# Kernel tuning notes

Hardware: AMD Instinct MI355X
Metric: run time of the kernel (lower is better)

Reference implementation:

```python
import jax, jax.numpy as jnp
import numpy as np

N, IN_DIM, H, D = 4096, 512, 8, 64
NEG = -1e9  # additive mask value for non-edges


def setup_inputs() -> dict:
    key = jax.random.key(0)
    k1, k2, k3, k4, k5, k6 = jax.random.split(key, 6)
    data = jax.random.normal(k1, (N, IN_DIM), dtype=jnp.float32)
    r = jax.random.uniform(k2, (N, N), dtype=jnp.float32)
    connectivity = jnp.where(r < 0.05, 0.0, NEG).astype(jnp.float32)
    # xavier-uniform-ish init for params
    lim_w = float(np.sqrt(6.0 / (IN_DIM + H * D)))
    W = jax.random.uniform(k3, (H * D, IN_DIM), jnp.float32, -lim_w, lim_w)
    b = jnp.zeros((H * D,), jnp.float32)
    lim_p = float(np.sqrt(6.0 / (H * D + 1)))
    src_proj = jax.random.uniform(k4, (1, H, D), jnp.float32, -lim_p, lim_p)
    trg_proj = jax.random.uniform(k5, (1, H, D), jnp.float32, -lim_p, lim_p)
    return {"data": data, "connectivity": connectivity, "W": W, "b": b,
            "src_proj": src_proj, "trg_proj": trg_proj}


def reference(data, connectivity, W, b, src_proj, trg_proj):
    # dropout is identity in eval mode (reference is deterministic)
    data1 = (data @ W.T + b).reshape(N, H, D)          # (N,H,D)
    src = jnp.einsum('nhd,xhd->nh', data1, src_proj)   # (N,H)
    trg = jnp.einsum('nhd,xhd->nh', data1, trg_proj)   # (N,H)
    # scores: (H,N,1) + (H,1,N) broadcast outer-sum
    e = src.T[:, :, None] + trg.T[:, None, :]          # (H,N,N)
    e = jnp.where(e >= 0, e, 0.01 * e)                 # LeakyReLU(0.01)
    e = e + connectivity[None, :, :]                   # additive mask
    scores = jax.nn.softmax(e, axis=-1)                # (H,N,N)
    # bmm over heads: (H,N,N) x (H,N,D) -> (H,N,D)
    out = jnp.einsum('hnm,hmd->hnd', scores, data1.transpose(1, 0, 2))
    out = out.transpose(1, 0, 2).reshape(N, H * D)     # concat=True
    return out
```

## Files before the change

kernel.cpp:

```cpp
#include <hip/hip_runtime.h>
#include <hip/hip_bf16.h>

#define NN 4096
#define IN_DIM 512
#define NH 8
#define DD 64
#define HD 512
#define QCAP 128
#define RCAP 448


typedef __attribute__((ext_vector_type(8))) short short8;
typedef __attribute__((ext_vector_type(4))) float f32x4;
typedef __attribute__((ext_vector_type(2))) float f32x2;

static __device__ __forceinline__ unsigned short f2bf(float x) {
    __hip_bfloat16 h = __float2bfloat16(x);
    return *reinterpret_cast<unsigned short*>(&h);
}

__global__ __launch_bounds__(256) void k_cast2(const float* __restrict__ inA,
                                               unsigned short* __restrict__ outA,
                                               int n4A,
                                               const float* __restrict__ inB,
                                               unsigned short* __restrict__ outB,
                                               int n4B) {
    int t = blockIdx.x * 256 + threadIdx.x;
    const float* in;
    unsigned short* out;
    if (t < n4A) {
        in = inA; out = outA;
    } else {
        t -= n4A;
        if (t >= n4B) return;
        in = inB; out = outB;
    }
    float4 v = ((const float4*)in)[t];
    ushort4 o;
    o.x = f2bf(v.x); o.y = f2bf(v.y); o.z = f2bf(v.z); o.w = f2bf(v.w);
    ((ushort4*)out)[t] = o;
}

__global__ __launch_bounds__(256) void k_gemm_fused(const unsigned short* __restrict__ Ab,
                                                    const unsigned short* __restrict__ Wb,
                                                    const float* __restrict__ bias,
                                                    const float* __restrict__ sp,
                                                    const float* __restrict__ tp,
                                                    unsigned short* __restrict__ Cb,
                                                    float* __restrict__ src,
                                                    float* __restrict__ trg) {
    const int lane = threadIdx.x & 63;
    const int w = threadIdx.x >> 6;
    const int col = lane & 15;
    const int quad = lane >> 4;
    const int koff = quad * 8;
    const int h = blockIdx.x;
    const int m0 = h * 64;
    const int n0 = blockIdx.y * 64;

    const short8* ap  = (const short8*)(Ab + (size_t)(n0 + w * 16 + col) * IN_DIM + koff);
    const short8* bp0 = (const short8*)(Wb + (size_t)(m0 +  0 + col) * IN_DIM + koff);
    const short8* bp1 = (const short8*)(Wb + (size_t)(m0 + 16 + col) * IN_DIM + koff);
    const short8* bp2 = (const short8*)(Wb + (size_t)(m0 + 32 + col) * IN_DIM + koff);
    const short8* bp3 = (const short8*)(Wb + (size_t)(m0 + 48 + col) * IN_DIM + koff);

    f32x4 acc0 = {0.f, 0.f, 0.f, 0.f}, acc1 = acc0, acc2 = acc0, acc3 = acc0;

#pragma unroll 4
    for (int ks = 0; ks < 16; ks++) {
        short8 a  = ap[ks * 4];
        short8 b0 = bp0[ks * 4];
        short8 b1 = bp1[ks * 4];
        short8 b2 = bp2[ks * 4];
        short8 b3 = bp3[ks * 4];
        acc0 = __builtin_amdgcn_mfma_f32_16x16x32_bf16(a, b0, acc0, 0, 0, 0);
        acc1 = __builtin_amdgcn_mfma_f32_16x16x32_bf16(a, b1, acc1, 0, 0, 0);
        acc2 = __builtin_amdgcn_mfma_f32_16x16x32_bf16(a, b2, acc2, 0, 0, 0);
        acc3 = __builtin_amdgcn_mfma_f32_16x16x32_bf16(a, b3, acc3, 0, 0, 0);
    }

    const int rbase = n0 + w * 16 + quad * 4;
    f32x4 accs[4] = {acc0, acc1, acc2, acc3};
    float ps[4] = {0.f, 0.f, 0.f, 0.f};
    float pt[4] = {0.f, 0.f, 0.f, 0.f};
#pragma unroll
    for (int mt = 0; mt < 4; mt++) {
        const int m = m0 + mt * 16 + col;
        const float bv  = bias[m];
        const float spv = sp[m];
        const float tpv = tp[m];
#pragma unroll
        for (int r = 0; r < 4; r++) {
            float v = accs[mt][r] + bv;
            Cb[(size_t)(rbase + r) * HD + m] = f2bf(v);
            ps[r] += v * spv;
            pt[r] += v * tpv;
        }
    }
#pragma unroll
    for (int off = 1; off <= 8; off <<= 1) {
#pragma unroll
        for (int r = 0; r < 4; r++) {
            ps[r] += __shfl_xor(ps[r], off, 64);
            pt[r] += __shfl_xor(pt[r], off, 64);
        }
    }
    if (col < 4)
        src[(rbase + col) * 8 + h] = ps[col];
    else if (col < 8)
        trg[(rbase + col - 4) * 8 + h] = pt[col - 4];
}

__global__ __launch_bounds__(256) void k_rowattn(const float* __restrict__ conn,
                                                 const float* __restrict__ src,
                                                 const float* __restrict__ trg,
                                                 const unsigned short* __restrict__ d1b,
                                                 float* __restrict__ out) {
    __shared__ unsigned short seg[4][QCAP];
    __shared__ unsigned short elist[RCAP + 8];
    __shared__ int wcnt[4];
    __shared__ float cbuf[3][64][9];
    const int w = threadIdx.x >> 6, lane = threadIdx.x & 63;
    const int i = blockIdx.x;
    const int h = lane >> 3, d8 = lane & 7;

    const float* crow = conn + (size_t)i * NN + w * 1024;
    int cnt = 0;
#pragma unroll
    for (int c0 = 0; c0 < 1024; c0 += 256) {
        float4 c = *(const float4*)(crow + c0 + lane * 4);
        float cv[4] = {c.x, c.y, c.z, c.w};
#pragma unroll
        for (int q = 0; q < 4; q++) {
            bool edge = (cv[q] == 0.0f);
            unsigned long long mask = __ballot(edge);
            int pre = __popcll(mask & ((1ull << lane) - 1ull));
            int pos = cnt + pre;
            if (edge && pos < QCAP)
                seg[w][pos] = (unsigned short)(w * 1024 + c0 + lane * 4 + q);
            cnt += __popcll(mask);
        }
    }
    if (cnt > QCAP) cnt = QCAP;
    if (lane == 0) wcnt[w] = cnt;
    __syncthreads();

    const int c0n = wcnt[0], c1n = wcnt[1], c2n = wcnt[2], c3n = wcnt[3];
    int tot = c0n + c1n + c2n + c3n;
    if (tot > RCAP) tot = RCAP;
    const int base = (w == 0) ? 0 : (w == 1) ? c0n
                   : (w == 2) ? c0n + c1n : c0n + c1n + c2n;
    for (int k = lane; k < cnt && base + k < RCAP; k += 64)
        elist[base + k] = seg[w][k];
    __syncthreads();
    if (threadIdx.x < 4)
        elist[tot + threadIdx.x] = (tot > 0) ? elist[tot - 1] : (unsigned short)0;
    __syncthreads();

    const float sh = src[i * 8 + h];
    const unsigned voffB = (unsigned)(h * 64 + d8 * 8) * 2u;
    const unsigned toffB = (unsigned)h << 2;
    const unsigned char* vb = (const unsigned char*)d1b;
    const unsigned char* tb = (const unsigned char*)trg;
    const int kbeg = (tot * w) >> 2;
    const int kend = (tot * (w + 1)) >> 2;

    f32x2 a01 = {0.f, 0.f}, a23 = a01, a45 = a01, a67 = a01;
    float lsum = 0.f;
    if (kend > kbeg) {
        unsigned j0 = elist[kbeg];
        unsigned j1 = elist[kbeg + 1];
        unsigned j2 = elist[kbeg + 2];
        float t0 = *(const float*)(tb + (j0 << 5) + toffB);
        float t1 = *(const float*)(tb + (j1 << 5) + toffB);
        uint4 U0 = *(const uint4*)(vb + (j0 << 10) + voffB);
        uint4 U1 = *(const uint4*)(vb + (j1 << 10) + voffB);
#pragma unroll 3
        for (int k = kbeg; k < kend; k++) {
            unsigned j3 = elist[k + 3];
            float t2 = *(const float*)(tb + (j2 << 5) + toffB);
            uint4 U2 = *(const uint4*)(vb + (j2 << 10) + voffB);
            float e = sh + t0;
            e = fmaxf(e, 0.01f * e);
            float p = __expf(e);
            lsum += p;
            f32x2 p2 = {p, p};
            f32x2 v01 = {__uint_as_float(U0.x << 16), __uint_as_float(U0.x & 0xffff0000u)};
            f32x2 v23 = {__uint_as_float(U0.y << 16), __uint_as_float(U0.y & 0xffff0000u)};
            f32x2 v45 = {__uint_as_float(U0.z << 16), __uint_as_float(U0.z & 0xffff0000u)};
            f32x2 v67 = {__uint_as_float(U0.w << 16), __uint_as_float(U0.w & 0xffff0000u)};
            a01 += p2 * v01;
            a23 += p2 * v23;
            a45 += p2 * v45;
            a67 += p2 * v67;
            t0 = t1; t1 = t2;
            U0 = U1; U1 = U2;
            j2 = j3;
        }
    }

    float acc[8] = {a01.x, a01.y, a23.x, a23.y, a45.x, a45.y, a67.x, a67.y};
    if (w > 0) {
#pragma unroll
        for (int r = 0; r < 8; r++) cbuf[w - 1][lane][r] = acc[r];
        cbuf[w - 1][lane][8] = lsum;
    }
    __syncthreads();
    if (w == 0) {
#pragma unroll
        for (int wv = 0; wv < 3; wv++) {
#pragma unroll
            for (int r = 0; r < 8; r++) acc[r] += cbuf[wv][lane][r];
            lsum += cbuf[wv][lane][8];
        }
        float inv = (lsum > 0.f) ? (1.f / lsum) : 0.f;
        float* op = out + (size_t)i * HD + h * 64 + d8 * 8;
        *(float4*)op = make_float4(acc[0] * inv, acc[1] * inv, acc[2] * inv, acc[3] * inv);
        *(float4*)(op + 4) = make_float4(acc[4] * inv, acc[5] * inv, acc[6] * inv, acc[7] * inv);
    }
}

extern "C" void kernel_launch(void* const* d_in, const int* in_sizes, int n_in,
                              void* d_out, int out_size, void* d_ws, size_t ws_size,
                              hipStream_t stream) {
    const float* data = (const float*)d_in[0];
    const float* conn = (const float*)d_in[1];
    const float* W    = (const float*)d_in[2];
    const float* bias = (const float*)d_in[3];
    const float* sp   = (const float*)d_in[4];
    const float* tp   = (const float*)d_in[5];
    float* out = (float*)d_out;

    unsigned short* d1b = (unsigned short*)d_ws;
    unsigned short* Ab  = d1b + (size_t)NN * HD;
    unsigned short* Wb  = Ab + (size_t)NN * IN_DIM;
    float* src  = (float*)(Wb + (size_t)HD * IN_DIM);
    float* trg  = src + NN * NH;

    const int n4A = NN * IN_DIM / 4;
    const int n4B = HD * IN_DIM / 4;
    k_cast2<<<dim3((n4A + n4B + 255) / 256), 256, 0, stream>>>(data, Ab, n4A, W, Wb, n4B);
    k_gemm_fused<<<dim3(NH, NN / 64), 256, 0, stream>>>(Ab, Wb, bias, sp, tp, d1b, src, trg);
    k_rowattn<<<dim3(NN), 256, 0, stream>>>(conn, src, trg, d1b, out);
}
```

Baseline: 168.3 us.

## Overlap connectivity bitmask scan with projection GEMM in one launch

The scan of the dense connectivity matrix moves out of the attention kernel into extra workgroups of the GEMM launch, where it builds a per-row 64x64-bit edge bitmask. The 64 MB mask read can then run alongside the GEMM. The attention kernel rebuilds its edge list from the bitmask with a prefix scan and ctz loop in one wave, and the old per-wave QCAP truncation is gone. src/trg are prescaled by log2(e) so the inner loop can use a native exp2. The cost is an extra bitmask buffer in workspace and a serial ctz loop per lane.

```diff
diff --git a/kernel.cpp b/kernel.cpp
--- a/kernel.cpp
+++ b/kernel.cpp
@@ -6,8 +6,10 @@
 #define NH 8
 #define DD 64
 #define HD 512
-#define QCAP 128
 #define RCAP 448
+#define GEMM_WGS 512
+#define SCAN_WGS 1024
+#define LOG2E 1.4426950408889634f
 
 
 typedef __attribute__((ext_vector_type(8))) short short8;
@@ -41,22 +43,39 @@
     ((ushort4*)out)[t] = o;
 }
 
-__global__ __launch_bounds__(256) void k_gemm_fused(const unsigned short* __restrict__ Ab,
-                                                    const unsigned short* __restrict__ Wb,
-                                                    const float* __restrict__ bias,
-                                                    const float* __restrict__ sp,
-                                                    const float* __restrict__ tp,
-                                                    unsigned short* __restrict__ Cb,
-                                                    float* __restrict__ src,
-                                                    float* __restrict__ trg) {
+__global__ __launch_bounds__(256) void k_gemm_scan(const unsigned short* __restrict__ Ab,
+                                                   const unsigned short* __restrict__ Wb,
+                                                   const float* __restrict__ bias,
+                                                   const float* __restrict__ sp,
+                                                   const float* __restrict__ tp,
+                                                   const float* __restrict__ conn,
+                                                   unsigned short* __restrict__ Cb,
+                                                   float* __restrict__ src,
+                                                   float* __restrict__ trg,
+                                                   unsigned long long* __restrict__ bm) {
     const int lane = threadIdx.x & 63;
     const int w = threadIdx.x >> 6;
+
+    if (blockIdx.x >= GEMM_WGS) {
+        const int row = (blockIdx.x - GEMM_WGS) * 4 + w;
+        const float* crow = conn + (size_t)row * NN;
+        unsigned long long keep = 0;
+#pragma unroll 8
+        for (int t = 0; t < 64; t++) {
+            float c = crow[t * 64 + lane];
+            unsigned long long m = __ballot(c == 0.0f);
+            if (lane == t) keep = m;
+        }
+        bm[(size_t)row * 64 + lane] = keep;
+        return;
+    }
+
     const int col = lane & 15;
     const int quad = lane >> 4;
     const int koff = quad * 8;
-    const int h = blockIdx.x;
+    const int h = blockIdx.x & 7;
     const int m0 = h * 64;
-    const int n0 = blockIdx.y * 64;
+    const int n0 = (blockIdx.x >> 3) * 64;
 
     const short8* ap  = (const short8*)(Ab + (size_t)(n0 + w * 16 + col) * IN_DIM + koff);
     const short8* bp0 = (const short8*)(Wb + (size_t)(m0 +  0 + col) * IN_DIM + koff);
@@ -106,56 +125,48 @@
         }
     }
     if (col < 4)
-        src[(rbase + col) * 8 + h] = ps[col];
+        src[(rbase + col) * 8 + h] = ps[col] * LOG2E;
     else if (col < 8)
-        trg[(rbase + col - 4) * 8 + h] = pt[col - 4];
-}
-
-__global__ __launch_bounds__(256) void k_rowattn(const float* __restrict__ conn,
+        trg[(rbase + col - 4) * 8 + h] = pt[col - 4] * LOG2E;
+}
+
+__global__ __launch_bounds__(256) void k_rowattn(const unsigned long long* __restrict__ bm,
                                                  const float* __restrict__ src,
                                                  const float* __restrict__ trg,
                                                  const unsigned short* __restrict__ d1b,
                                                  float* __restrict__ out) {
-    __shared__ unsigned short seg[4][QCAP];
     __shared__ unsigned short elist[RCAP + 8];
-    __shared__ int wcnt[4];
+    __shared__ int sTot;
     __shared__ float cbuf[3][64][9];
     const int w = threadIdx.x >> 6, lane = threadIdx.x & 63;
     const int i = blockIdx.x;
     const int h = lane >> 3, d8 = lane & 7;
 
-    const float* crow = conn + (size_t)i * NN + w * 1024;
-    int cnt = 0;
-#pragma unroll
-    for (int c0 = 0; c0 < 1024; c0 += 256) {
-        float4 c = *(const float4*)(crow + c0 + lane * 4);
-        float cv[4] = {c.x, c.y, c.z, c.w};
-#pragma unroll
-        for (int q = 0; q < 4; q++) {
-            bool edge = (cv[q] == 0.0f);
-            unsigned long long mask = __ballot(edge);
-            int pre = __popcll(mask & ((1ull << lane) - 1ull));
-            int pos = cnt + pre;
-            if (edge && pos < QCAP)
-                seg[w][pos] = (unsigned short)(w * 1024 + c0 + lane * 4 + q);
-            cnt += __popcll(mask);
-        }
-    }
-    if (cnt > QCAP) cnt = QCAP;
-    if (lane == 0) wcnt[w] = cnt;
+    if (threadIdx.x < 64) {
+        unsigned long long m = bm[(size_t)i * 64 + lane];
+        const int cnt = __popcll(m);
+        int pre = cnt;
+#pragma unroll
+        for (int off = 1; off < 64; off <<= 1) {
+            int v = __shfl_up(pre, off, 64);
+            if (lane >= off) pre += v;
+        }
+        int tot = __shfl(pre, 63, 64);
+        int pos = pre - cnt;
+        const int base = lane * 64;
+        while (m) {
+            int b = __builtin_ctzll(m);
+            m &= m - 1;
+            if (pos < RCAP) elist[pos] = (unsigned short)(base + b);
+            pos++;
+        }
+        if (tot > RCAP) tot = RCAP;
+        unsigned short sv = (tot > 0) ? elist[tot - 1] : (unsigned short)0;
+        if (lane < 8) elist[tot + lane] = sv;
+        if (lane == 0) sTot = tot;
+    }
     __syncthreads();
-
-    const int c0n = wcnt[0], c1n = wcnt[1], c2n = wcnt[2], c3n = wcnt[3];
-    int tot = c0n + c1n + c2n + c3n;
-    if (tot > RCAP) tot = RCAP;
-    const int base = (w == 0) ? 0 : (w == 1) ? c0n
-                   : (w == 2) ? c0n + c1n : c0n + c1n + c2n;
-    for (int k = lane; k < cnt && base + k < RCAP; k += 64)
-        elist[base + k] = seg[w][k];
-    __syncthreads();
-    if (threadIdx.x < 4)
-        elist[tot + threadIdx.x] = (tot > 0) ? elist[tot - 1] : (unsigned short)0;
-    __syncthreads();
+    const int tot = sTot;
 
     const float sh = src[i * 8 + h];
     const unsigned voffB = (unsigned)(h * 64 + d8 * 8) * 2u;
@@ -182,7 +193,7 @@
             uint4 U2 = *(const uint4*)(vb + (j2 << 10) + voffB);
             float e = sh + t0;
             e = fmaxf(e, 0.01f * e);
-            float p = __expf(e);
+            float p = __builtin_amdgcn_exp2f(e);
             lsum += p;
             f32x2 p2 = {p, p};
             f32x2 v01 = {__uint_as_float(U0.x << 16), __uint_as_float(U0.x & 0xffff0000u)};
@@ -236,10 +247,12 @@
     unsigned short* Wb  = Ab + (size_t)NN * IN_DIM;
     float* src  = (float*)(Wb + (size_t)HD * IN_DIM);
     float* trg  = src + NN * NH;
+    unsigned long long* bm = (unsigned long long*)(trg + NN * NH);
 
     const int n4A = NN * IN_DIM / 4;
     const int n4B = HD * IN_DIM / 4;
     k_cast2<<<dim3((n4A + n4B + 255) / 256), 256, 0, stream>>>(data, Ab, n4A, W, Wb, n4B);
-    k_gemm_fused<<<dim3(NH, NN / 64), 256, 0, stream>>>(Ab, Wb, bias, sp, tp, d1b, src, trg);
-    k_rowattn<<<dim3(NN), 256, 0, stream>>>(conn, src, trg, d1b, out);
-}
+    k_gemm_scan<<<dim3(GEMM_WGS + SCAN_WGS), 256, 0, stream>>>(Ab, Wb, bias, sp, tp, conn,
+                                                               d1b, src, trg, bm);
+    k_rowattn<<<dim3(NN), 256, 0, stream>>>(bm, src, trg, d1b, out);
+}
```

Measured after the change: 169.0 us. About the same (+0.4%).
